# Kernel tuning notes

Hardware: AMD Instinct MI355X
Metric: run time of the kernel (lower is better)

## Reference

```python
import jax, jax.numpy as jnp
import numpy as np

K = 3        # num patches
S = 2        # scale factor
G = 32       # base glimpse size


def _avg_pool(x, k):
    # x: (b, c, H, W), kernel=stride=k (matches F.avg_pool2d(x, k))
    if k == 1:
        return x
    b, c, h, w = x.shape
    return x.reshape(b, c, h // k, k, w // k, k).mean(axis=(3, 5))


def _extract_patch(x, l, size):
    # x: (b, c, h, w); l: (b, 2) in [-1, 1]; returns (b, c, size, size)
    b, c, h, w = x.shape
    start = (0.5 * ((l + 1.0) * h)).astype(jnp.int32)  # (b, 2) [col, row]
    pad = size // 2 + 1
    xp = jnp.pad(x, ((0, 0), (0, 0), (pad, pad), (pad, pad)))

    def slice_one(img, st):
        # img: (c, hp, wp); st: (2,) -> rows use st[1], cols use st[0]
        return jax.lax.dynamic_slice(img, (0, st[1], st[0]), (c, size, size))

    return jax.vmap(slice_one)(xp, start)


def _foveate(x, l):
    phi = []
    size = G
    for _ in range(K):
        phi.append(_extract_patch(x, l, size))
        size = int(S * size)
    # pool every coarser patch back to GxG, concat on channel, flatten
    phi = [_avg_pool(p, p.shape[-1] // G) for p in phi]
    phi = jnp.concatenate(phi, axis=1)          # (b, K*c, G, G)
    return phi.reshape(phi.shape[0], -1)        # (b, K*c*G*G)


def setup_inputs() -> dict:
    key = jax.random.key(0)
    ks = jax.random.split(key, 10)
    b, c, h, w = 256, 3, 224, 224
    h_g = h_l = 1024
    dim = K * G * G * c  # 9216
    x = jax.random.normal(ks[0], (b, c, h, w), dtype=jnp.float32)
    l_prev = jax.random.uniform(ks[1], (b, 2), dtype=jnp.float32, minval=-1.0, maxval=1.0)
    def lin(k, fan_in, fan_out):
        return jax.random.normal(k, (fan_in, fan_out), dtype=jnp.float32) / np.sqrt(fan_in)
    return {
        "x": x, "l_prev": l_prev,
        "W1": lin(ks[2], dim, h_g), "b1": jnp.zeros((h_g,), jnp.float32),
        "W2": lin(ks[3], 2, h_l),   "b2": jnp.zeros((h_l,), jnp.float32),
        "W3": lin(ks[4], h_g, h_g + h_l), "b3": jnp.zeros((h_g + h_l,), jnp.float32),
        "W4": lin(ks[5], h_l, h_g + h_l), "b4": jnp.zeros((h_g + h_l,), jnp.float32),
    }


def reference(x, l_prev, W1, b1, W2, b2, W3, b3, W4, b4):
    glimpse = _foveate(x, l_prev)                       # (b, K*c*G*G)
    g_out = jax.nn.relu(glimpse @ W1 + b1)              # (b, h_g)
    l_out = jax.nn.relu(l_prev @ W2 + b2)               # (b, h_l)
    what = g_out @ W3 + b3                              # (b, h_g+h_l)
    where = l_out @ W4 + b4                             # (b, h_g+h_l)
    return jax.nn.relu(what + where)
```

## Files before the change

kernel.cpp:

```cpp
#include <hip/hip_runtime.h>

typedef __bf16 bf16_t;
typedef __bf16 bf16x8 __attribute__((ext_vector_type(8)));
typedef float f32x4 __attribute__((ext_vector_type(4)));
typedef unsigned short us4 __attribute__((ext_vector_type(4)));
typedef unsigned short us8 __attribute__((ext_vector_type(8)));

__global__ __launch_bounds__(256) void foveate2(const float* __restrict__ x,
                                                const float* __restrict__ l,
                                                bf16_t* __restrict__ g)
{
  __shared__ float R[128 * 128];
  const int b = blockIdx.x, ch = blockIdx.y;
  const float l0 = l[2 * b], l1 = l[2 * b + 1];
  const int st0 = (int)(0.5f * ((l0 + 1.0f) * 224.0f));
  const int st1 = (int)(0.5f * ((l1 + 1.0f) * 224.0f));
  const int r0 = st1 - 65, c0 = st0 - 65;
  const float* xc = x + ((size_t)b * 3 + ch) * 50176;

  for (int it = 0; it < 64; ++it) {
    const int p = it * 256 + threadIdx.x;
    const int r = p >> 7, c = p & 127;
    const int gr = r0 + r, gc = c0 + c;
    float v = 0.0f;
    if ((unsigned)gr < 224u && (unsigned)gc < 224u) v = xc[gr * 224 + gc];
    R[p] = v;
  }
  __syncthreads();

  bf16_t* gb = g + (size_t)b * 9216 + ch * 1024;
  for (int it = 0; it < 4; ++it) {
    const int q = it * 256 + threadIdx.x;
    const int gy = q >> 5, gx = q & 31;
    gb[q] = (bf16_t)R[(48 + gy) * 128 + 48 + gx];
  }
  for (int it = 0; it < 4; ++it) {
    const int q = it * 256 + threadIdx.x;
    const int gy = q >> 5, gx = q & 31;
    const int base = (32 + 2 * gy) * 128 + 32 + 2 * gx;
    const float s = R[base] + R[base + 1] + R[base + 128] + R[base + 129];
    gb[3072 + q] = (bf16_t)(s * 0.25f);
  }
  for (int it = 0; it < 4; ++it) {
    const int q = it * 256 + threadIdx.x;
    const int gy = q >> 5, gx = q & 31;
    float s = 0.0f;
#pragma unroll
    for (int dy = 0; dy < 4; ++dy) {
      const f32x4 v = *(const f32x4*)&R[(4 * gy + dy) * 128 + 4 * gx];
      s += v[0] + v[1] + v[2] + v[3];
    }
    gb[6144 + q] = (bf16_t)(s * 0.0625f);
  }
}

template<int WAVES, int BN, int KCHUNK, int NDIM, int KFULL, int KB1>
__global__ __launch_bounds__(WAVES * 64) void gemm_direct(const bf16_t* __restrict__ A,
                                                          const float* __restrict__ Bp0,
                                                          const float* __restrict__ Bp1,
                                                          float* __restrict__ part)
{
  constexpr int SM = 2;
  constexpr int SN = BN / 16;
  constexpr int M = WAVES * 32;
  const int t = threadIdx.x, w = t >> 6, lane = t & 63;
  const int lr = lane & 15, kg = lane >> 4;
  const int bn0 = blockIdx.y * BN;
  const int ks0 = blockIdx.z * KCHUNK;
  const int m0 = w * 32;

  f32x4 acc[SM][SN] = {};
#pragma unroll 2
  for (int k0 = 0; k0 < KCHUNK; k0 += 32) {
    const int kbase = ks0 + k0;
    const float* brow = (kbase < KB1) ? (Bp0 + (size_t)kbase * NDIM)
                                      : (Bp1 + (size_t)(kbase - KB1) * NDIM);
    bf16x8 af[SM];
#pragma unroll
    for (int sm = 0; sm < SM; ++sm)
      af[sm] = __builtin_bit_cast(bf16x8,
          *(const us8*)(A + (size_t)(m0 + sm * 16 + lr) * KFULL + kbase + kg * 8));
    bf16x8 bfr[SN];
#pragma unroll
    for (int sn = 0; sn < SN; ++sn) {
      const float* bp = brow + (size_t)(kg * 8) * NDIM + bn0 + sn * 16 + lr;
#pragma unroll
      for (int j = 0; j < 8; ++j) bfr[sn][j] = (bf16_t)bp[(size_t)j * NDIM];
    }
#pragma unroll
    for (int sm = 0; sm < SM; ++sm)
#pragma unroll
      for (int sn = 0; sn < SN; ++sn)
        acc[sm][sn] = __builtin_amdgcn_mfma_f32_16x16x32_bf16(af[sm], bfr[sn], acc[sm][sn], 0, 0, 0);
  }
  float* outp = part + (size_t)blockIdx.z * ((size_t)M * NDIM);
#pragma unroll
  for (int sm = 0; sm < SM; ++sm)
#pragma unroll
    for (int sn = 0; sn < SN; ++sn)
#pragma unroll
      for (int r = 0; r < 4; ++r) {
        const int gm = m0 + sm * 16 + kg * 4 + r;
        const int gn = bn0 + sn * 16 + lr;
        outp[(size_t)gm * NDIM + gn] = acc[sm][sn][r];
      }
}

__global__ __launch_bounds__(256) void fuse_mid(const float* __restrict__ part1,
                                                const float* __restrict__ b1,
                                                const float* __restrict__ lprev,
                                                const float* __restrict__ W2,
                                                const float* __restrict__ b2,
                                                bf16_t* __restrict__ A2)
{
  const int e = (blockIdx.x * 256 + threadIdx.x) * 4;
  const int row = e >> 11, col = e & 2047;
  f32x4 s;
  if (col < 1024) {
    s = *(const f32x4*)(b1 + col);
#pragma unroll
    for (int z = 0; z < 16; ++z)
      s += *(const f32x4*)(part1 + (size_t)z * 262144 + row * 1024 + col);
  } else {
    const int n = col - 1024;
    const f32x4 w0 = *(const f32x4*)(W2 + n);
    const f32x4 w1 = *(const f32x4*)(W2 + 1024 + n);
    s = *(const f32x4*)(b2 + n) + lprev[2 * row] * w0 + lprev[2 * row + 1] * w1;
  }
  us4 o;
#pragma unroll
  for (int j = 0; j < 4; ++j)
    o[j] = __builtin_bit_cast(unsigned short, (bf16_t)fmaxf(s[j], 0.0f));
  *(us4*)(A2 + e) = o;
}

__global__ __launch_bounds__(256) void epilogue2(const float* __restrict__ part2,
                                                 const float* __restrict__ b3,
                                                 const float* __restrict__ b4,
                                                 float* __restrict__ out)
{
  const int e = (blockIdx.x * 256 + threadIdx.x) * 4;
  const int col = e & 2047;
  f32x4 s = *(const f32x4*)(b3 + col) + *(const f32x4*)(b4 + col);
#pragma unroll
  for (int z = 0; z < 8; ++z)
    s += *(const f32x4*)(part2 + (size_t)z * 524288 + e);
  f32x4 o;
#pragma unroll
  for (int j = 0; j < 4; ++j) o[j] = fmaxf(s[j], 0.0f);
  *(f32x4*)(out + e) = o;
}

extern "C" void kernel_launch(void* const* d_in, const int* in_sizes, int n_in,
                              void* d_out, int out_size, void* d_ws, size_t ws_size,
                              hipStream_t stream)
{
  const float* x     = (const float*)d_in[0];
  const float* lprev = (const float*)d_in[1];
  const float* W1    = (const float*)d_in[2];
  const float* b1    = (const float*)d_in[3];
  const float* W2    = (const float*)d_in[4];
  const float* b2    = (const float*)d_in[5];
  const float* W3    = (const float*)d_in[6];
  const float* b3    = (const float*)d_in[7];
  const float* W4    = (const float*)d_in[8];
  const float* b4    = (const float*)d_in[9];
  float* out = (float*)d_out;

  char* ws = (char*)d_ws;
  bf16_t* glimpse = (bf16_t*)ws;
  bf16_t* A2      = (bf16_t*)(ws + 4718592);
  float*  part1   = (float*)(ws + 5767168);
  float*  part2   = (float*)(ws + 22544384);

  foveate2<<<dim3(256, 3), 256, 0, stream>>>(x, lprev, glimpse);
  gemm_direct<8, 64, 576, 1024, 9216, 9216>
      <<<dim3(1, 16, 16), 512, 0, stream>>>(glimpse, W1, W1, part1);
  fuse_mid<<<512, 256, 0, stream>>>(part1, b1, lprev, W2, b2, A2);
  gemm_direct<8, 64, 256, 2048, 2048, 1024>
      <<<dim3(1, 32, 8), 512, 0, stream>>>(A2, W3, W4, part2);
  epilogue2<<<512, 256, 0, stream>>>(part2, b3, b4, out);
}
```

Measured before the change: 327.4 us.

## Stage converted B tile in shared memory shared across waves in GEMMs

The GEMM kernel now cooperatively loads each 32x64 fp32 B tile once per block, converts pairs to packed bf16 and stores them in padded LDS. Each wave then reads its MFMA B fragments from LDS instead of every wave re-reading the same B elements from global memory with strided scalar loads. This removes eightfold redundant B traffic. In exchange it adds two block barriers per k-step and has no double buffering, so there is less overlap of loads and compute.

Result: no change. 332.1 us (+1.4%).

```diff
diff --git a/kernel.cpp b/kernel.cpp
--- a/kernel.cpp
+++ b/kernel.cpp
@@ -5,6 +5,8 @@
 typedef float f32x4 __attribute__((ext_vector_type(4)));
 typedef unsigned short us4 __attribute__((ext_vector_type(4)));
 typedef unsigned short us8 __attribute__((ext_vector_type(8)));
+typedef unsigned int u32x2 __attribute__((ext_vector_type(2)));
+typedef unsigned int u32x4 __attribute__((ext_vector_type(4)));
 
 __global__ __launch_bounds__(256) void foveate2(const float* __restrict__ x,
                                                 const float* __restrict__ l,
@@ -55,43 +57,61 @@
 }
 
 template<int WAVES, int BN, int KCHUNK, int NDIM, int KFULL, int KB1>
-__global__ __launch_bounds__(WAVES * 64) void gemm_direct(const bf16_t* __restrict__ A,
-                                                          const float* __restrict__ Bp0,
-                                                          const float* __restrict__ Bp1,
-                                                          float* __restrict__ part)
+__global__ __launch_bounds__(WAVES * 64) void gemm_bpack(const bf16_t* __restrict__ A,
+                                                         const float* __restrict__ Bp0,
+                                                         const float* __restrict__ Bp1,
+                                                         float* __restrict__ part)
 {
   constexpr int SM = 2;
   constexpr int SN = BN / 16;
   constexpr int M = WAVES * 32;
+  constexpr int LDB = 18;
+  __shared__ unsigned int Bl[BN * LDB];
   const int t = threadIdx.x, w = t >> 6, lane = t & 63;
   const int lr = lane & 15, kg = lane >> 4;
   const int bn0 = blockIdx.y * BN;
   const int ks0 = blockIdx.z * KCHUNK;
   const int m0 = w * 32;
+  const int sn_n = t & 63;
+  const int sk2 = (t >> 6) * 2;
 
   f32x4 acc[SM][SN] = {};
-#pragma unroll 2
+
   for (int k0 = 0; k0 < KCHUNK; k0 += 32) {
     const int kbase = ks0 + k0;
-    const float* brow = (kbase < KB1) ? (Bp0 + (size_t)kbase * NDIM)
-                                      : (Bp1 + (size_t)(kbase - KB1) * NDIM);
+    const float* bbase = (kbase < KB1) ? (Bp0 + (size_t)kbase * NDIM)
+                                       : (Bp1 + (size_t)(kbase - KB1) * NDIM);
     bf16x8 af[SM];
 #pragma unroll
     for (int sm = 0; sm < SM; ++sm)
       af[sm] = __builtin_bit_cast(bf16x8,
           *(const us8*)(A + (size_t)(m0 + sm * 16 + lr) * KFULL + kbase + kg * 8));
+#pragma unroll
+    for (int i = 0; i < 2; ++i) {
+      const int k2 = sk2 + i, k = 2 * k2;
+      const float a0 = bbase[(size_t)k * NDIM + bn0 + sn_n];
+      const float a1 = bbase[(size_t)(k + 1) * NDIM + bn0 + sn_n];
+      const unsigned int p =
+          (unsigned int)__builtin_bit_cast(unsigned short, (bf16_t)a0) |
+          ((unsigned int)__builtin_bit_cast(unsigned short, (bf16_t)a1) << 16);
+      Bl[sn_n * LDB + k2] = p;
+    }
+    __syncthreads();
     bf16x8 bfr[SN];
 #pragma unroll
     for (int sn = 0; sn < SN; ++sn) {
-      const float* bp = brow + (size_t)(kg * 8) * NDIM + bn0 + sn * 16 + lr;
-#pragma unroll
-      for (int j = 0; j < 8; ++j) bfr[sn][j] = (bf16_t)bp[(size_t)j * NDIM];
+      const unsigned int* p = &Bl[(sn * 16 + lr) * LDB + kg * 4];
+      const u32x2 d0 = *(const u32x2*)p;
+      const u32x2 d1 = *(const u32x2*)(p + 2);
+      const u32x4 c = {d0[0], d0[1], d1[0], d1[1]};
+      bfr[sn] = __builtin_bit_cast(bf16x8, c);
     }
 #pragma unroll
     for (int sm = 0; sm < SM; ++sm)
 #pragma unroll
       for (int sn = 0; sn < SN; ++sn)
         acc[sm][sn] = __builtin_amdgcn_mfma_f32_16x16x32_bf16(af[sm], bfr[sn], acc[sm][sn], 0, 0, 0);
+    __syncthreads();
   }
   float* outp = part + (size_t)blockIdx.z * ((size_t)M * NDIM);
 #pragma unroll
@@ -174,10 +194,10 @@
   float*  part2   = (float*)(ws + 22544384);
 
   foveate2<<<dim3(256, 3), 256, 0, stream>>>(x, lprev, glimpse);
-  gemm_direct<8, 64, 576, 1024, 9216, 9216>
+  gemm_bpack<8, 64, 576, 1024, 9216, 9216>
       <<<dim3(1, 16, 16), 512, 0, stream>>>(glimpse, W1, W1, part1);
   fuse_mid<<<512, 256, 0, stream>>>(part1, b1, lprev, W2, b2, A2);
-  gemm_direct<8, 64, 256, 2048, 2048, 1024>
+  gemm_bpack<8, 64, 256, 2048, 2048, 1024>
       <<<dim3(1, 32, 8), 512, 0, stream>>>(A2, W3, W4, part2);
   epilogue2<<<512, 256, 0, stream>>>(part2, b3, b4, out);
 }
```
